# Kernel optimization log

Hardware: AMD Instinct MI355X
Metric: run time of the kernel (lower is better)

## Reference

```python
import jax, jax.numpy as jnp
import numpy as np

N, E = 50000, 800000
F_NODE, F_EDGE, HID, EMB, HEADS = 128, 16, 64, 32, 4
BN_EPS = 1e-5


def _glorot(key, shape):
    fan_in = shape[0] if len(shape) > 1 else shape[-1]
    return jax.random.normal(key, shape, jnp.float32) / np.sqrt(fan_in)


def setup_inputs() -> dict:
    key = jax.random.key(0)
    ks = jax.random.split(key, 32)
    inp = {
        "x": jax.random.normal(ks[0], (N, F_NODE), jnp.float32),
        "edge_attr": jax.random.normal(ks[1], (E, F_EDGE), jnp.float32),
        # GAT layer 0: in=F_NODE, heads=4, C=HID
        "W0": _glorot(ks[2], (F_NODE, HEADS * HID)),
        "We0": _glorot(ks[3], (F_EDGE, HEADS * HID)),
        "as0": _glorot(ks[4], (HEADS, HID)),
        "ad0": _glorot(ks[5], (HEADS, HID)),
        "ae0": _glorot(ks[6], (HEADS, HID)),
        "b0": jnp.zeros((HEADS * HID,), jnp.float32),
        "bn0_g": jnp.ones((HEADS * HID,), jnp.float32),
        "bn0_b": jnp.zeros((HEADS * HID,), jnp.float32),
        # GAT layer 1: in=HEADS*HID, heads=1, C=EMB
        "W1": _glorot(ks[7], (HEADS * HID, EMB)),
        "We1": _glorot(ks[8], (F_EDGE, EMB)),
        "as1": _glorot(ks[9], (1, EMB)),
        "ad1": _glorot(ks[10], (1, EMB)),
        "ae1": _glorot(ks[11], (1, EMB)),
        "b1": jnp.zeros((EMB,), jnp.float32),
        # node decoder: 32 -> 128 -> 64 -> 128
        "ndW1": _glorot(ks[12], (EMB, 2 * HID)),   "ndb1": jnp.zeros((2 * HID,), jnp.float32),
        "nd_g": jnp.ones((2 * HID,), jnp.float32), "nd_b": jnp.zeros((2 * HID,), jnp.float32),
        "ndW2": _glorot(ks[13], (2 * HID, HID)),   "ndb2": jnp.zeros((HID,), jnp.float32),
        "ndW3": _glorot(ks[14], (HID, F_NODE)),    "ndb3": jnp.zeros((F_NODE,), jnp.float32),
        # edge decoder: 2*32+16=80 -> 128 -> 64 -> 1
        "edW1": _glorot(ks[15], (2 * EMB + F_EDGE, 2 * HID)), "edb1": jnp.zeros((2 * HID,), jnp.float32),
        "ed_g": jnp.ones((2 * HID,), jnp.float32), "ed_b": jnp.zeros((2 * HID,), jnp.float32),
        "edW2": _glorot(ks[16], (2 * HID, HID)),   "edb2": jnp.zeros((HID,), jnp.float32),
        "edW3": _glorot(ks[17], (HID, 1)),         "edb3": jnp.zeros((1,), jnp.float32),
        "edge_index": jax.random.randint(ks[18], (2, E), 0, N, jnp.int64),
    }
    return inp


def _bn(x, g, b):
    # eval-mode BatchNorm1d with running mean 0, var 1
    return x / np.sqrt(1.0 + BN_EPS) * g + b


def _gat(x, edge_index, edge_attr, W, b, We, att_s, att_d, att_e, heads, C):
    n = x.shape[0]
    src, dst = edge_index[0], edge_index[1]
    e = edge_attr.shape[0]
    # add self loops; self-loop edge_attr = scatter-mean of incoming edge_attr (PyG fill_value='mean')
    esum = jax.ops.segment_sum(edge_attr, dst, num_segments=n)
    cnt = jax.ops.segment_sum(jnp.ones((e,), edge_attr.dtype), dst, num_segments=n)
    loop_attr = esum / jnp.maximum(cnt, 1.0)[:, None]
    loop = jnp.arange(n, dtype=src.dtype)
    src_f = jnp.concatenate([src, loop])
    dst_f = jnp.concatenate([dst, loop])
    ea = jnp.concatenate([edge_attr, loop_attr], axis=0)
    xw = (x @ W).reshape(n, heads, C)                       # [N,H,C]
    a_s = (xw * att_s).sum(-1)                              # [N,H]
    a_d = (xw * att_d).sum(-1)
    a_e = ((ea @ We).reshape(-1, heads, C) * att_e).sum(-1)  # [E+N,H]
    alpha = jax.nn.leaky_relu(a_s[src_f] + a_d[dst_f] + a_e, 0.2)
    # segment softmax over destination neighborhoods
    m = jax.ops.segment_max(alpha, dst_f, num_segments=n)
    alpha = jnp.exp(alpha - m[dst_f])
    s = jax.ops.segment_sum(alpha, dst_f, num_segments=n)
    alpha = alpha / (s[dst_f] + 1e-16)
    out = jax.ops.segment_sum(alpha[:, :, None] * xw[src_f], dst_f, num_segments=n)
    return out.reshape(n, heads * C) + b


def reference(x, edge_attr, W0, b0, We0, as0, ad0, ae0, bn0_g, bn0_b,
              W1, b1, We1, as1, ad1, ae1,
              ndW1, ndb1, nd_g, nd_b, ndW2, ndb2, ndW3, ndb3,
              edW1, edb1, ed_g, ed_b, edW2, edb2, edW3, edb3,
              edge_index):
    # encoder
    h = _gat(x, edge_index, edge_attr, W0, b0, We0, as0, ad0, ae0, HEADS, HID)
    h = jax.nn.elu(_bn(h, bn0_g, bn0_b))  # residual skipped: 256 != 128; dropout is eval-mode identity
    z = _gat(h, edge_index, edge_attr, W1, b1, We1, as1, ad1, ae1, 1, EMB)
    # node decoder
    n1 = _bn(jax.nn.relu(z @ ndW1 + ndb1), nd_g, nd_b)
    node_recon = jax.nn.relu(n1 @ ndW2 + ndb2) @ ndW3 + ndb3
    # edge decoder
    src, dst = edge_index[0], edge_index[1]
    ef = jnp.concatenate([z[src], z[dst], edge_attr], axis=1)  # [E, 2*EMB+F_EDGE]
    e1 = _bn(jax.nn.relu(ef @ edW1 + edb1), ed_g, ed_b)
    edge_recon = jax.nn.sigmoid((jax.nn.relu(e1 @ edW2 + edb2) @ edW3 + edb3)).squeeze(-1)
    return (z, node_recon, edge_recon)
```

## Files before the change

kernel.cpp:

```cpp
#include <hip/hip_runtime.h>
#include <math.h>

#define BN_K 0.9999950000374997f

static __device__ __forceinline__ float lrelu02(float x) { return x > 0.f ? x : 0.2f * x; }

typedef _Float16 half8 __attribute__((ext_vector_type(8)));
typedef __fp16 fp16x2 __attribute__((ext_vector_type(2)));
typedef float f32x4 __attribute__((ext_vector_type(4)));

static __device__ __forceinline__ unsigned short f2h(float x)
{
    union { _Float16 h; unsigned short u; } q;
    q.h = (_Float16)x;
    return q.u;
}
static __device__ __forceinline__ float h2f(unsigned short u)
{
    union { unsigned short u; _Float16 h; } q;
    q.u = u;
    return (float)q.h;
}
static __device__ __forceinline__ unsigned pkrtz(float a, float b)
{
    union { fp16x2 h; unsigned u; } q;
    q.h = __builtin_amdgcn_cvt_pkrtz(a, b);
    return q.u;
}

__global__ void k_ae_vec(const float* __restrict__ We0, const float* __restrict__ ae0,
                         const float* __restrict__ We1, const float* __restrict__ ae1,
                         const float* __restrict__ edbb, const float* __restrict__ edW2,
                         const float* __restrict__ edb2,
                         float* __restrict__ v0, float* __restrict__ v1,
                         float* __restrict__ b2p)
{
    int t = threadIdx.x;
    if (t < 64) {
        int h = t >> 4, k = t & 15;
        float s = 0.f;
        for (int c = 0; c < 64; ++c) s += We0[k * 256 + h * 64 + c] * ae0[h * 64 + c];
        v0[h * 16 + k] = s;
    } else if (t < 80) {
        int k = t - 64;
        float s = 0.f;
        for (int c = 0; c < 32; ++c) s += We1[k * 32 + c] * ae1[c];
        v1[k] = s;
    } else if (t < 144) {
        int n = t - 80;
        float s = 0.f;
        for (int k = 0; k < 128; ++k) s += edbb[k] * edW2[k * 64 + n];
        b2p[n] = edb2[n] + s;
    }
}

__global__ void k_deg_count(const int* __restrict__ dst, int* __restrict__ deg, int E)
{
    int e = blockIdx.x * blockDim.x + threadIdx.x;
    if (e < E) atomicAdd(&deg[dst[e]], 1);
}

#define SCHUNK 4096
__global__ __launch_bounds__(1024) void k_scan1(const int* __restrict__ deg,
                                                int* __restrict__ rowptr,
                                                int* __restrict__ bsum, int n)
{
    __shared__ int sbuf[1024];
    int b = blockIdx.x, t = threadIdx.x;
    int i0 = b * SCHUNK + t * 4;
    int v[4];
#pragma unroll
    for (int j = 0; j < 4; ++j) v[j] = (i0 + j < n) ? deg[i0 + j] + 1 : 0;
    int s = v[0] + v[1] + v[2] + v[3];
    sbuf[t] = s;
    __syncthreads();
    for (int d = 1; d < 1024; d <<= 1) {
        int tmp = (t >= d) ? sbuf[t - d] : 0;
        __syncthreads();
        sbuf[t] += tmp;
        __syncthreads();
    }
    int run = sbuf[t] - s;
#pragma unroll
    for (int j = 0; j < 4; ++j) {
        run += v[j];
        if (i0 + j < n) rowptr[i0 + j + 1] = run;
    }
    if (t == 1023) bsum[b] = sbuf[1023];
    if (b == 0 && t == 0) rowptr[0] = 0;
}

__global__ void k_scan3(const int* __restrict__ bsum, const int* __restrict__ deg,
                        int* __restrict__ rowptr, int* __restrict__ cur, int n)
{
    int i = blockIdx.x * blockDim.x + threadIdx.x;
    if (i >= n) return;
    int chunk = i / SCHUNK;
    int off = 0;
    for (int b = 0; b < chunk; ++b) off += bsum[b];
    int r = rowptr[i + 1] + off;
    rowptr[i + 1] = r;
    cur[i] = r - (deg[i] + 1);
}

__global__ void k_fill(const int* __restrict__ dst, int* __restrict__ cur,
                       int* __restrict__ col, int E, int N)
{
    int t = blockIdx.x * blockDim.x + threadIdx.x;
    if (t >= E + N) return;
    int d = (t < E) ? dst[t] : (t - E);
    int slot = atomicAdd(&cur[d], 1);
    col[slot] = t;
}

__global__ __launch_bounds__(256) void k_loop_mean(
    const int* __restrict__ rowptr, const int* __restrict__ col,
    const unsigned short* __restrict__ ea16,
    const float* __restrict__ v0, const float* __restrict__ v1,
    float* __restrict__ a_e0, float* __restrict__ a_e1, int N, int E)
{
    int wv = threadIdx.x >> 6, lane = threadIdx.x & 63;
    int i = blockIdx.x * 4 + wv;
    if (i >= N) return;
    int beg = rowptr[i], end = rowptr[i + 1];
    int q = lane >> 4, k = lane & 15;
    float sum = 0.f;
    for (int p = beg + q; p < end; p += 4) {
        int eid = col[p];
        if (eid < E) sum += h2f(ea16[(size_t)eid * 16 + k]);
    }
    sum += __shfl_xor(sum, 16);
    sum += __shfl_xor(sum, 32);
    int cnt = end - beg - 1;
    float mean = sum / (float)max(cnt, 1);
    float p0 = mean * v0[q * 16 + k];
    float p1 = mean * v1[k];
#pragma unroll
    for (int mm = 1; mm < 16; mm <<= 1) { p0 += __shfl_xor(p0, mm); p1 += __shfl_xor(p1, mm); }
    if (k == 0) a_e0[(size_t)(E + i) * 4 + q] = p0;
    if (lane == 0) a_e1[E + i] = p1;
}

__global__ void k_edge_ae(const float* __restrict__ ea,
                          const float* __restrict__ v0, const float* __restrict__ v1,
                          float* __restrict__ a_e0, float* __restrict__ a_e1,
                          unsigned short* __restrict__ ea16, int E)
{
    int idx = blockIdx.x * blockDim.x + threadIdx.x;
    if (idx >= E) return;
    const float* row = ea + (size_t)idx * 16;
    float r[16];
#pragma unroll
    for (int k = 0; k < 16; ++k) r[k] = row[k];
#pragma unroll
    for (int h = 0; h < 4; ++h) {
        float s = 0.f;
#pragma unroll
        for (int k = 0; k < 16; ++k) s = fmaf(r[k], v0[h * 16 + k], s);
        a_e0[(size_t)idx * 4 + h] = s;
    }
    float s1 = 0.f;
#pragma unroll
    for (int k = 0; k < 16; ++k) s1 = fmaf(r[k], v1[k], s1);
    a_e1[idx] = s1;
#pragma unroll
    for (int k = 0; k < 16; k += 4) {
        ushort4 o;
        o.x = f2h(r[k]); o.y = f2h(r[k + 1]); o.z = f2h(r[k + 2]); o.w = f2h(r[k + 3]);
        *(ushort4*)(ea16 + (size_t)idx * 16 + k) = o;
    }
}

__global__ __launch_bounds__(512) void k_pack_all(
    const float* __restrict__ W0, const float* __restrict__ W1,
    const float* __restrict__ nd1, const float* __restrict__ nd2, const float* __restrict__ nd3,
    const float* __restrict__ ed1, const float* __restrict__ ed2,
    const float* __restrict__ edb1, const float* __restrict__ edg,
    unsigned short* __restrict__ pw)
{
    int f = blockIdx.x, t = threadIdx.x;
    int l = t >> 3, i = t & 7, g = l >> 4, m = l & 15;
    float v;
    if (f < 64) {
        int q = f; int k = 32 * (q >> 4) + 8 * g + i, n = 16 * (q & 15) + m;
        v = W0[(size_t)k * 256 + n];
    } else if (f < 80) {
        int q = f - 64; int k = 32 * (q >> 1) + 8 * g + i, n = 16 * (q & 1) + m;
        v = W1[(size_t)k * 32 + n];
    } else if (f < 88) {
        int q = f - 80; int k = 8 * g + i, n = 16 * q + m;
        v = nd1[(size_t)k * 128 + n];
    } else if (f < 104) {
        int q = f - 88; int k = 32 * (q >> 2) + 8 * g + i, n = 16 * (q & 3) + m;
        v = nd2[(size_t)k * 64 + n];
    } else if (f < 120) {
        int q = f - 104; int k = 32 * (q >> 3) + 8 * g + i, n = 16 * (q & 7) + m;
        v = nd3[(size_t)k * 128 + n];
    } else if (f < 144) {
        int q = f - 120; int k = 32 * (q >> 3) + 8 * g + i, n = 16 * (q & 7) + m;
        v = (k < 80) ? ed1[(size_t)k * 128 + n] : (k == 80 ? edb1[n] : 0.f);
    } else {
        int q = f - 144; int k = 32 * (q >> 2) + 8 * g + i, n = 16 * (q & 3) + m;
        v = ed2[(size_t)k * 64 + n] * (edg[k] * BN_K);
    }
    pw[(size_t)f * 512 + t] = f2h(v);
}

template <int KC, int NT, int MODE, int AF32, int NTOT, int DOTS>
__global__ __launch_bounds__(256) void k_gemm16(
    const void* __restrict__ Ain, const unsigned short* __restrict__ pwB,
    void* __restrict__ outp, int M,
    const float* __restrict__ bias, const float* __restrict__ g_,
    const float* __restrict__ bb_,
    const float* __restrict__ attS, const float* __restrict__ attD,
    float* __restrict__ a_sO, float* __restrict__ a_dO)
{
    constexpr int K = KC * 32;
    constexpr int LDA = K + 8;
    __shared__ unsigned short s_pw[KC * NT * 512];
    __shared__ unsigned short s_a[64 * LDA];
    __shared__ float s_c[3 * NT * 16];

    int t = threadIdx.x;
    int ttoff = blockIdx.y * NT;
    for (int idx = t; idx < KC * NT * 64; idx += 256) {
        int f = idx >> 6, e8 = idx & 63;
        int c = f / NT, tt = f - c * NT;
        *(half8*)&s_pw[(size_t)idx * 8] =
            *(const half8*)&pwB[(((size_t)(c * NTOT + ttoff + tt)) * 64 + e8) * 8];
    }
    if (MODE) {
        for (int c = t; c < NT * 16; c += 256) {
            s_c[c] = bias[ttoff * 16 + c];
            if (MODE == 2) {
                s_c[NT * 16 + c] = g_[ttoff * 16 + c] * BN_K;
                s_c[2 * NT * 16 + c] = bb_[ttoff * 16 + c];
            }
        }
    }
    int wv = t >> 6, lane = t & 63, gq = lane >> 4, m = lane & 15;

    float asv[NT], adv[NT];
    if (DOTS) {
#pragma unroll
        for (int tt = 0; tt < NT; ++tt) {
            asv[tt] = attS[ttoff * 16 + 16 * tt + m];
            adv[tt] = attD[ttoff * 16 + 16 * tt + m];
        }
    }

    int nrt = (M + 63) >> 6;
    for (int rt = blockIdx.x; rt < nrt; rt += gridDim.x) {
        int r0 = rt << 6;
        __syncthreads();
        for (int idx = t; idx < 64 * (K / 8); idx += 256) {
            int row = idx / (K / 8), cb = idx % (K / 8);
            half8 v = {};
            if (r0 + row < M) {
                if (AF32) {
                    const float* Af = (const float*)Ain + (size_t)(r0 + row) * K + cb * 8;
                    float4 u0 = *(const float4*)Af;
                    float4 u1 = *(const float4*)(Af + 4);
                    union { half8 h; unsigned u[4]; } q;
                    q.u[0] = pkrtz(u0.x, u0.y); q.u[1] = pkrtz(u0.z, u0.w);
                    q.u[2] = pkrtz(u1.x, u1.y); q.u[3] = pkrtz(u1.z, u1.w);
                    v = q.h;
                } else {
                    v = *(const half8*)&((const unsigned short*)Ain)[(size_t)(r0 + row) * K + cb * 8];
                }
            }
            *(half8*)&s_a[row * LDA + cb * 8] = v;
        }
        __syncthreads();
        f32x4 acc[NT] = {};
#pragma unroll
        for (int c = 0; c < KC; ++c) {
            half8 a = *(half8*)&s_a[(wv * 16 + m) * LDA + 32 * c + 8 * gq];
#pragma unroll
            for (int tt = 0; tt < NT; ++tt) {
                half8 b = *(const half8*)&s_pw[(c * NT + tt) * 512 + lane * 8];
                acc[tt] = __builtin_amdgcn_mfma_f32_16x16x32_f16(a, b, acc[tt], 0, 0, 0);
            }
        }
#pragma unroll
        for (int tt = 0; tt < NT; ++tt) {
            int col = 16 * tt + m;
            int ocol = ttoff * 16 + col;
            float cb = MODE ? s_c[col] : 0.f;
#pragma unroll
            for (int r = 0; r < 4; ++r) {
                int row = r0 + wv * 16 + 4 * gq + r;
                float v = acc[tt][r] + cb;
                if (MODE == 1) v = fmaxf(v, 0.f);
                if (MODE == 2) v = fmaxf(v, 0.f) * s_c[NT * 16 + col] + s_c[2 * NT * 16 + col];
                if (MODE == 3) {
                    if (row < M) ((float*)outp)[(size_t)row * (NTOT * 16) + ocol] = v;
                } else {
                    float o = __shfl_xor(v, 1);
                    if (!(m & 1) && row < M)
                        *(unsigned*)&((unsigned short*)outp)[(size_t)row * (NTOT * 16) + ocol] =
                            pkrtz(v, o);
                }
            }
        }
        if (DOTS == 1) {
#pragma unroll
            for (int r = 0; r < 4; ++r) {
                float psA = 0.f, pdA = 0.f, psB = 0.f, pdB = 0.f;
#pragma unroll
                for (int tt = 0; tt < NT && tt < 4; ++tt) {
                    psA = fmaf(acc[tt][r], asv[tt], psA);
                    pdA = fmaf(acc[tt][r], adv[tt], pdA);
                }
#pragma unroll
                for (int tt = 4; tt < NT; ++tt) {
                    psB = fmaf(acc[tt][r], asv[tt], psB);
                    pdB = fmaf(acc[tt][r], adv[tt], pdB);
                }
#pragma unroll
                for (int mm = 1; mm < 16; mm <<= 1) {
                    psA += __shfl_xor(psA, mm); pdA += __shfl_xor(pdA, mm);
                    psB += __shfl_xor(psB, mm); pdB += __shfl_xor(pdB, mm);
                }
                int row = r0 + wv * 16 + 4 * gq + r;
                if (m == 0 && row < M) {
                    int hA = 2 * blockIdx.y;
                    a_sO[(size_t)row * 4 + hA] = psA; a_sO[(size_t)row * 4 + hA + 1] = psB;
                    a_dO[(size_t)row * 4 + hA] = pdA; a_dO[(size_t)row * 4 + hA + 1] = pdB;
                }
            }
        } else if (DOTS == 2) {
#pragma unroll
            for (int r = 0; r < 4; ++r) {
                float ps = 0.f, pd = 0.f;
#pragma unroll
                for (int tt = 0; tt < NT; ++tt) {
                    ps = fmaf(acc[tt][r], asv[tt], ps);
                    pd = fmaf(acc[tt][r], adv[tt], pd);
                }
#pragma unroll
                for (int mm = 1; mm < 16; mm <<= 1) {
                    ps += __shfl_xor(ps, mm); pd += __shfl_xor(pd, mm);
                }
                int row = r0 + wv * 16 + 4 * gq + r;
                if (m == 0 && row < M) { a_sO[row] = ps; a_dO[row] = pd; }
            }
        }
    }
}

__global__ __launch_bounds__(64) void k_gat0_agg(
    const int* __restrict__ rowptr, const int* __restrict__ col, const int* __restrict__ srcA,
    const float* __restrict__ a_s, const float* __restrict__ a_d, const float* __restrict__ a_e,
    const unsigned short* __restrict__ xw16, const float* __restrict__ b0,
    const float* __restrict__ bng, const float* __restrict__ bnb,
    unsigned short* __restrict__ hout16, int N, int E)
{
    int i = blockIdx.x;
    int lane = threadIdx.x;
    int beg = rowptr[i], end = rowptr[i + 1];
    float ad[4];
#pragma unroll
    for (int h = 0; h < 4; ++h) ad[h] = a_d[(size_t)i * 4 + h];

    float al[4] = {-1e30f, -1e30f, -1e30f, -1e30f};
    int sl0 = i;
    int p0 = beg + lane;
    if (p0 < end) {
        int eid = col[p0];
        sl0 = (eid < E) ? srcA[eid] : i;
        float4 as4 = *(const float4*)(a_s + (size_t)sl0 * 4);
        float4 ae4 = *(const float4*)(a_e + (size_t)eid * 4);
        al[0] = lrelu02(as4.x + ad[0] + ae4.x);
        al[1] = lrelu02(as4.y + ad[1] + ae4.y);
        al[2] = lrelu02(as4.z + ad[2] + ae4.z);
        al[3] = lrelu02(as4.w + ad[3] + ae4.w);
    }
    float mx[4] = {al[0], al[1], al[2], al[3]};
    for (int p = p0 + 64; p < end; p += 64) {
        int eid = col[p];
        int s = (eid < E) ? srcA[eid] : i;
        float4 as4 = *(const float4*)(a_s + (size_t)s * 4);
        float4 ae4 = *(const float4*)(a_e + (size_t)eid * 4);
        mx[0] = fmaxf(mx[0], lrelu02(as4.x + ad[0] + ae4.x));
        mx[1] = fmaxf(mx[1], lrelu02(as4.y + ad[1] + ae4.y));
        mx[2] = fmaxf(mx[2], lrelu02(as4.z + ad[2] + ae4.z));
        mx[3] = fmaxf(mx[3], lrelu02(as4.w + ad[3] + ae4.w));
    }
#pragma unroll
    for (int h = 0; h < 4; ++h)
#pragma unroll
        for (int m = 1; m < 64; m <<= 1) mx[h] = fmaxf(mx[h], __shfl_xor(mx[h], m));

    __shared__ float wls[256];
    __shared__ int s_src[64];
    int hl = lane >> 4;
    float accx = 0.f, accy = 0.f, accz = 0.f, accw = 0.f;
    float s0 = 0.f, s1 = 0.f, s2 = 0.f, s3 = 0.f;
    for (int base = beg; base < end; base += 64) {
        int p = base + lane;
        int cnt = min(64, end - base);
        if (p < end) {
            float aa0, aa1, aa2, aa3;
            int s;
            if (base == beg) {
                s = sl0;
                aa0 = al[0]; aa1 = al[1]; aa2 = al[2]; aa3 = al[3];
            } else {
                int eid = col[p];
                s = (eid < E) ? srcA[eid] : i;
                float4 as4 = *(const float4*)(a_s + (size_t)s * 4);
                float4 ae4 = *(const float4*)(a_e + (size_t)eid * 4);
                aa0 = lrelu02(as4.x + ad[0] + ae4.x);
                aa1 = lrelu02(as4.y + ad[1] + ae4.y);
                aa2 = lrelu02(as4.z + ad[2] + ae4.z);
                aa3 = lrelu02(as4.w + ad[3] + ae4.w);
            }
            float w0 = expf(aa0 - mx[0]);
            float w1 = expf(aa1 - mx[1]);
            float w2 = expf(aa2 - mx[2]);
            float w3 = expf(aa3 - mx[3]);
            s0 += w0; s1 += w1; s2 += w2; s3 += w3;
            wls[lane * 4 + 0] = w0; wls[lane * 4 + 1] = w1;
            wls[lane * 4 + 2] = w2; wls[lane * 4 + 3] = w3;
            s_src[lane] = s;
        }
        __syncthreads();
        int q = 0;
        for (; q + 3 < cnt; q += 4) {
            int ss0 = s_src[q], ss1 = s_src[q + 1], ss2 = s_src[q + 2], ss3 = s_src[q + 3];
            ushort4 x0 = *(const ushort4*)(xw16 + (size_t)ss0 * 256 + lane * 4);
            ushort4 x1 = *(const ushort4*)(xw16 + (size_t)ss1 * 256 + lane * 4);
            ushort4 x2 = *(const ushort4*)(xw16 + (size_t)ss2 * 256 + lane * 4);
            ushort4 x3 = *(const ushort4*)(xw16 + (size_t)ss3 * 256 + lane * 4);
            float w0 = wls[q * 4 + hl], w1 = wls[(q + 1) * 4 + hl];
            float w2 = wls[(q + 2) * 4 + hl], w3 = wls[(q + 3) * 4 + hl];
            accx = fmaf(w0, h2f(x0.x), accx); accy = fmaf(w0, h2f(x0.y), accy);
            accz = fmaf(w0, h2f(x0.z), accz); accw = fmaf(w0, h2f(x0.w), accw);
            accx = fmaf(w1, h2f(x1.x), accx); accy = fmaf(w1, h2f(x1.y), accy);
            accz = fmaf(w1, h2f(x1.z), accz); accw = fmaf(w1, h2f(x1.w), accw);
            accx = fmaf(w2, h2f(x2.x), accx); accy = fmaf(w2, h2f(x2.y), accy);
            accz = fmaf(w2, h2f(x2.z), accz); accw = fmaf(w2, h2f(x2.w), accw);
            accx = fmaf(w3, h2f(x3.x), accx); accy = fmaf(w3, h2f(x3.y), accy);
            accz = fmaf(w3, h2f(x3.z), accz); accw = fmaf(w3, h2f(x3.w), accw);
        }
        for (; q < cnt; ++q) {
            int ss = s_src[q];
            float w = wls[q * 4 + hl];
            ushort4 xv = *(const ushort4*)(xw16 + (size_t)ss * 256 + lane * 4);
            accx = fmaf(w, h2f(xv.x), accx);
            accy = fmaf(w, h2f(xv.y), accy);
            accz = fmaf(w, h2f(xv.z), accz);
            accw = fmaf(w, h2f(xv.w), accw);
        }
        __syncthreads();
    }
#pragma unroll
    for (int m = 1; m < 64; m <<= 1) {
        s0 += __shfl_xor(s0, m); s1 += __shfl_xor(s1, m);
        s2 += __shfl_xor(s2, m); s3 += __shfl_xor(s3, m);
    }
    float sden = ((hl == 0) ? s0 : (hl == 1) ? s1 : (hl == 2) ? s2 : s3) + 1e-16f;

    int ch = lane * 4;
    float out[4] = {accx / sden, accy / sden, accz / sden, accw / sden};
    ushort4 ov;
    unsigned short* po = (unsigned short*)&ov;
#pragma unroll
    for (int j = 0; j < 4; ++j) {
        int c = ch + j;
        float v = out[j] + b0[c];
        v = v * (BN_K * bng[c]) + bnb[c];
        po[j] = f2h((v > 0.f) ? v : expm1f(v));
    }
    *(ushort4*)(hout16 + (size_t)i * 256 + ch) = ov;
}

__global__ __launch_bounds__(64) void k_gat1_agg(
    const int* __restrict__ rowptr, const int* __restrict__ col, const int* __restrict__ srcA,
    const float* __restrict__ a_s, const float* __restrict__ a_d, const float* __restrict__ a_e,
    const unsigned short* __restrict__ xw16, const float* __restrict__ b1,
    float* __restrict__ zout, unsigned short* __restrict__ z16, int N, int E)
{
    int i = blockIdx.x;
    int lane = threadIdx.x;
    int beg = rowptr[i], end = rowptr[i + 1];
    float ad = a_d[i];
    float al = -1e30f;
    int sl0 = i;
    int p0 = beg + lane;
    if (p0 < end) {
        int eid = col[p0];
        sl0 = (eid < E) ? srcA[eid] : i;
        al = lrelu02(a_s[sl0] + ad + a_e[eid]);
    }
    float mx = al;
    for (int p = p0 + 64; p < end; p += 64) {
        int eid = col[p];
        int s = (eid < E) ? srcA[eid] : i;
        mx = fmaxf(mx, lrelu02(a_s[s] + ad + a_e[eid]));
    }
#pragma unroll
    for (int m = 1; m < 64; m <<= 1) mx = fmaxf(mx, __shfl_xor(mx, m));

    __shared__ float wls[64];
    __shared__ int s_src[64];
    float accA = 0.f, accB = 0.f, ssum = 0.f;
    int sub = lane >> 4;
    int ch = (lane & 15) * 2;
    for (int base = beg; base < end; base += 64) {
        int p = base + lane;
        int cnt = min(64, end - base);
        if (p < end) {
            float aa;
            int s;
            if (base == beg) { s = sl0; aa = al; }
            else {
                int eid = col[p];
                s = (eid < E) ? srcA[eid] : i;
                aa = lrelu02(a_s[s] + ad + a_e[eid]);
            }
            float w = expf(aa - mx);
            ssum += w;
            wls[lane] = w;
            s_src[lane] = s;
        }
        __syncthreads();
        int q = sub;
        for (; q + 12 < cnt; q += 16) {
            int ss0 = s_src[q], ss1 = s_src[q + 4], ss2 = s_src[q + 8], ss3 = s_src[q + 12];
            float w0 = wls[q], w1 = wls[q + 4], w2 = wls[q + 8], w3 = wls[q + 12];
            ushort2 x0 = *(const ushort2*)(xw16 + (size_t)ss0 * 32 + ch);
            ushort2 x1 = *(const ushort2*)(xw16 + (size_t)ss1 * 32 + ch);
            ushort2 x2 = *(const ushort2*)(xw16 + (size_t)ss2 * 32 + ch);
            ushort2 x3 = *(const ushort2*)(xw16 + (size_t)ss3 * 32 + ch);
            accA = fmaf(w0, h2f(x0.x), accA); accB = fmaf(w0, h2f(x0.y), accB);
            accA = fmaf(w1, h2f(x1.x), accA); accB = fmaf(w1, h2f(x1.y), accB);
            accA = fmaf(w2, h2f(x2.x), accA); accB = fmaf(w2, h2f(x2.y), accB);
            accA = fmaf(w3, h2f(x3.x), accA); accB = fmaf(w3, h2f(x3.y), accB);
        }
        for (; q < cnt; q += 4) {
            int ss = s_src[q];
            float w = wls[q];
            ushort2 xv = *(const ushort2*)(xw16 + (size_t)ss * 32 + ch);
            accA = fmaf(w, h2f(xv.x), accA);
            accB = fmaf(w, h2f(xv.y), accB);
        }
        __syncthreads();
    }
#pragma unroll
    for (int m = 1; m < 64; m <<= 1) ssum += __shfl_xor(ssum, m);
    accA += __shfl_xor(accA, 16); accB += __shfl_xor(accB, 16);
    accA += __shfl_xor(accA, 32); accB += __shfl_xor(accB, 32);
    if (lane < 16) {
        float inv = 1.f / (ssum + 1e-16f);
        float vA = accA * inv + b1[ch];
        float vB = accB * inv + b1[ch + 1];
        *(float2*)(zout + (size_t)i * 32 + ch) = make_float2(vA, vB);
        *(unsigned*)(z16 + (size_t)i * 32 + ch) = pkrtz(vA, vB);
    }
}

#define H1_STRIDE 136

__global__ __launch_bounds__(256, 3) void k_edge_dec_mfma(
    const unsigned short* __restrict__ z16, const unsigned short* __restrict__ ea16,
    const int* __restrict__ srcA, const int* __restrict__ dstA,
    const unsigned short* __restrict__ pw,
    const float* __restrict__ b2p, const float* __restrict__ w3,
    const float* __restrict__ b3v, float* __restrict__ out, int E)
{
    __shared__ unsigned short s_pw[24 * 512];
    __shared__ unsigned short s_h1[4][16 * H1_STRIDE];

    int t = threadIdx.x;
    for (int idx = t; idx < 1536; idx += 256)
        *(half8*)&s_pw[idx * 8] = *(const half8*)&pw[idx * 8];
    __syncthreads();

    int wv = t >> 6, lane = t & 63;
    int g = lane >> 4, m = lane & 15;
    unsigned short* h1 = s_h1[wv];

    half8 w2r[16];
#pragma unroll
    for (int q = 0; q < 16; ++q)
        w2r[q] = *(const half8*)&pw[(size_t)(24 + q) * 512 + lane * 8];

    float w3t[4], b2t[4];
#pragma unroll
    for (int q = 0; q < 4; ++q) { w3t[q] = w3[16 * q + m]; b2t[q] = b2p[16 * q + m]; }
    float b3 = b3v[0];

    int ntiles = (E + 15) >> 4;
    int gw = blockIdx.x * 4 + wv;
    int nw = gridDim.x * 4;

    half8 a0n = {}, a1n = {}, a2n = {};
    {
        int e = (gw << 4) + m;
        if (gw < ntiles && e < E) {
            int si = srcA[e], di = dstA[e];
            a0n = *(const half8*)&z16[(size_t)si * 32 + 8 * g];
            a1n = *(const half8*)&z16[(size_t)di * 32 + 8 * g];
            if (g < 2) a2n = *(const half8*)&ea16[(size_t)e * 16 + 8 * g];
        }
        if (g == 2) a2n[0] = (_Float16)1.f;
    }

    for (int tile = gw; tile < ntiles; ) {
        half8 a0 = a0n, a1 = a1n, a2 = a2n;
        int e0 = tile << 4;
        int nxt = tile + nw;

        a0n = half8{}; a1n = half8{}; a2n = half8{};
        {
            int e = (nxt << 4) + m;
            if (nxt < ntiles && e < E) {
                int si = srcA[e], di = dstA[e];
                a0n = *(const half8*)&z16[(size_t)si * 32 + 8 * g];
                a1n = *(const half8*)&z16[(size_t)di * 32 + 8 * g];
                if (g < 2) a2n = *(const half8*)&ea16[(size_t)e * 16 + 8 * g];
            }
            if (g == 2) a2n[0] = (_Float16)1.f;
        }

        f32x4 acc1[8] = {};
#pragma unroll
        for (int tt = 0; tt < 8; ++tt)
            acc1[tt] = __builtin_amdgcn_mfma_f32_16x16x32_f16(a0, *(const half8*)&s_pw[(0 * 8 + tt) * 512 + lane * 8], acc1[tt], 0, 0, 0);
#pragma unroll
        for (int tt = 0; tt < 8; ++tt)
            acc1[tt] = __builtin_amdgcn_mfma_f32_16x16x32_f16(a1, *(const half8*)&s_pw[(1 * 8 + tt) * 512 + lane * 8], acc1[tt], 0, 0, 0);
#pragma unroll
        for (int tt = 0; tt < 8; ++tt)
            acc1[tt] = __builtin_amdgcn_mfma_f32_16x16x32_f16(a2, *(const half8*)&s_pw[(2 * 8 + tt) * 512 + lane * 8], acc1[tt], 0, 0, 0);

#pragma unroll
        for (int tt = 0; tt < 8; ++tt) {
#pragma unroll
            for (int r = 0; r < 4; ++r) {
                float v = fmaxf(acc1[tt][r], 0.f);
                float vo = __shfl_xor(v, 1);
                if (!(m & 1))
                    *(unsigned*)&h1[(4 * g + r) * H1_STRIDE + 16 * tt + m] = pkrtz(v, vo);
            }
        }
        asm volatile("s_waitcnt lgkmcnt(0)" ::: "memory");
        __builtin_amdgcn_sched_barrier(0);

        f32x4 acc2[4] = {};
#pragma unroll
        for (int c = 0; c < 4; ++c) {
            half8 a = *(half8*)&h1[m * H1_STRIDE + 32 * c + 8 * g];
#pragma unroll
            for (int tt = 0; tt < 4; ++tt)
                acc2[tt] = __builtin_amdgcn_mfma_f32_16x16x32_f16(a, w2r[c * 4 + tt], acc2[tt], 0, 0, 0);
        }
        float s[4];
#pragma unroll
        for (int r = 0; r < 4; ++r) {
            float acc = 0.f;
#pragma unroll
            for (int tt = 0; tt < 4; ++tt) {
                float v = fmaxf(acc2[tt][r] + b2t[tt], 0.f);
                acc = fmaf(v, w3t[tt], acc);
            }
            acc += __shfl_xor(acc, 1);
            acc += __shfl_xor(acc, 2);
            acc += __shfl_xor(acc, 4);
            acc += __shfl_xor(acc, 8);
            s[r] = acc;
        }
        if (m == 0) {
            int eb = e0 + 4 * g;
            if (eb + 3 < E) {
                float4 o;
                o.x = 1.f / (1.f + expf(-(s[0] + b3)));
                o.y = 1.f / (1.f + expf(-(s[1] + b3)));
                o.z = 1.f / (1.f + expf(-(s[2] + b3)));
                o.w = 1.f / (1.f + expf(-(s[3] + b3)));
                *(float4*)(out + eb) = o;
            } else {
#pragma unroll
                for (int r = 0; r < 4; ++r)
                    if (eb + r < E) out[eb + r] = 1.f / (1.f + expf(-(s[r] + b3)));
            }
        }
        tile = nxt;
    }
}

extern "C" void kernel_launch(void* const* d_in, const int* in_sizes, int n_in,
                              void* d_out, int out_size, void* d_ws, size_t ws_size,
                              hipStream_t stream)
{
    const float* x    = (const float*)d_in[0];
    const float* ea   = (const float*)d_in[1];
    const float* W0   = (const float*)d_in[2];
    const float* We0  = (const float*)d_in[3];
    const float* as0  = (const float*)d_in[4];
    const float* ad0  = (const float*)d_in[5];
    const float* ae0  = (const float*)d_in[6];
    const float* b0   = (const float*)d_in[7];
    const float* bn0g = (const float*)d_in[8];
    const float* bn0b = (const float*)d_in[9];
    const float* W1   = (const float*)d_in[10];
    const float* We1  = (const float*)d_in[11];
    const float* as1  = (const float*)d_in[12];
    const float* ad1  = (const float*)d_in[13];
    const float* ae1  = (const float*)d_in[14];
    const float* b1   = (const float*)d_in[15];
    const float* ndW1 = (const float*)d_in[16];
    const float* ndb1 = (const float*)d_in[17];
    const float* ndg  = (const float*)d_in[18];
    const float* ndbb = (const float*)d_in[19];
    const float* ndW2 = (const float*)d_in[20];
    const float* ndb2 = (const float*)d_in[21];
    const float* ndW3 = (const float*)d_in[22];
    const float* ndb3 = (const float*)d_in[23];
    const float* edW1 = (const float*)d_in[24];
    const float* edb1 = (const float*)d_in[25];
    const float* edg  = (const float*)d_in[26];
    const float* edbb = (const float*)d_in[27];
    const float* edW2 = (const float*)d_in[28];
    const float* edb2 = (const float*)d_in[29];
    const float* edW3 = (const float*)d_in[30];
    const float* edb3 = (const float*)d_in[31];
    const int*   eidx = (const int*)d_in[32];

    const int N = in_sizes[0] / 128;
    const int E = in_sizes[1] / 16;
    const int* srcA = eidx;
    const int* dstA = eidx + E;

    char* ws = (char*)d_ws;
    size_t o = 0;
    auto alloc = [&](size_t bytes) -> void* {
        void* p = ws + o;
        o = (o + bytes + 255) & ~(size_t)255;
        return p;
    };
    typedef unsigned short u16;
    u16*   xw0_16 = (u16*)alloc((size_t)N * 256 * 2);
    u16*   hbuf16 = (u16*)alloc((size_t)N * 256 * 2);
    u16*   xw1_16 = (u16*)alloc((size_t)N * 32 * 2);
    u16*   z16    = (u16*)alloc((size_t)N * 32 * 2);
    u16*   n1_16  = (u16*)alloc((size_t)N * 128 * 2);
    u16*   h2n16  = (u16*)alloc((size_t)N * 64 * 2);
    u16*   ea16   = (u16*)alloc((size_t)E * 16 * 2);
    float* a_s0   = (float*)alloc((size_t)N * 4 * 4);
    float* a_d0   = (float*)alloc((size_t)N * 4 * 4);
    float* a_e0a  = (float*)alloc((size_t)(E + N) * 4 * 4);
    float* a_e1a  = (float*)alloc((size_t)(E + N) * 4);
    float* a_s1   = (float*)alloc((size_t)N * 4);
    float* a_d1   = (float*)alloc((size_t)N * 4);
    int*   deg    = (int*)alloc((size_t)N * 4);
    int*   rowptr = (int*)alloc((size_t)(N + 1) * 4);
    int*   cur    = (int*)alloc((size_t)N * 4);
    int*   col    = (int*)alloc((size_t)(E + N) * 4);
    int*   bsum   = (int*)alloc(64 * 4);
    float* v0     = (float*)alloc(64 * 4);
    float* v1     = (float*)alloc(16 * 4);
    float* b2p    = (float*)alloc(64 * 4);
    u16*   pw     = (u16*)alloc((size_t)160 * 512 * 2);

    float* z_out    = (float*)d_out;
    float* node_out = z_out + (size_t)N * 32;
    float* edge_out = node_out + (size_t)N * 128;

    const int nb = (N + SCHUNK - 1) / SCHUNK;
    const int nrt = (N + 63) / 64;

    hipMemsetAsync(deg, 0, (size_t)N * 4, stream);
    k_pack_all<<<160, 512, 0, stream>>>(W0, W1, ndW1, ndW2, ndW3, edW1, edW2, edb1, edg, pw);
    k_ae_vec<<<1, 192, 0, stream>>>(We0, ae0, We1, ae1, edbb, edW2, edb2, v0, v1, b2p);
    k_deg_count<<<(E + 255) / 256, 256, 0, stream>>>(dstA, deg, E);
    k_scan1<<<nb, 1024, 0, stream>>>(deg, rowptr, bsum, N);
    k_scan3<<<(N + 255) / 256, 256, 0, stream>>>(bsum, deg, rowptr, cur, N);
    k_fill<<<(E + N + 255) / 256, 256, 0, stream>>>(dstA, cur, col, E, N);
    k_edge_ae<<<(E + 255) / 256, 256, 0, stream>>>(ea, v0, v1, a_e0a, a_e1a, ea16, E);
    k_loop_mean<<<(N + 3) / 4, 256, 0, stream>>>(rowptr, col, ea16, v0, v1, a_e0a, a_e1a, N, E);

    k_gemm16<4, 8, 0, 1, 16, 1><<<dim3(nrt, 2), 256, 0, stream>>>(
        x, pw, xw0_16, N, nullptr, nullptr, nullptr, as0, ad0, a_s0, a_d0);
    k_gat0_agg<<<N, 64, 0, stream>>>(rowptr, col, srcA, a_s0, a_d0, a_e0a, xw0_16, b0, bn0g, bn0b,
                                     hbuf16, N, E);

    k_gemm16<8, 2, 0, 0, 2, 2><<<dim3(nrt, 1), 256, 0, stream>>>(
        hbuf16, pw + (size_t)64 * 512, xw1_16, N, nullptr, nullptr, nullptr,
        as1, ad1, a_s1, a_d1);
    k_gat1_agg<<<N, 64, 0, stream>>>(rowptr, col, srcA, a_s1, a_d1, a_e1a, xw1_16, b1,
                                     z_out, z16, N, E);

    k_gemm16<1, 8, 2, 0, 8, 0><<<dim3(nrt, 1), 256, 0, stream>>>(
        z16, pw + (size_t)80 * 512, n1_16, N, ndb1, ndg, ndbb, nullptr, nullptr, nullptr, nullptr);
    k_gemm16<4, 4, 1, 0, 4, 0><<<dim3(nrt, 1), 256, 0, stream>>>(
        n1_16, pw + (size_t)88 * 512, h2n16, N, ndb2, nullptr, nullptr, nullptr, nullptr, nullptr, nullptr);
    k_gemm16<2, 8, 3, 0, 8, 0><<<dim3(nrt, 1), 256, 0, stream>>>(
        h2n16, pw + (size_t)104 * 512, node_out, N, ndb3, nullptr, nullptr, nullptr, nullptr, nullptr, nullptr);

    k_edge_dec_mfma<<<768, 256, 0, stream>>>(z16, ea16, srcA, dstA, pw + (size_t)120 * 512,
                                             b2p, edW3, edb3, edge_out, E);
}
```

Baseline: 424.9 us.

## Fuse node decoder MLP into one MFMA kernel and merge setup kernels

Replaces the three node-decoder GEMM launches with a single persistent kernel that keeps intermediate n1 and h2 activations in shared memory as fp16 and chains three MFMA stages per 64-row tile. Also folds the degree-count atomics into the edge attention-prep kernel and moves the small attention-vector precompute into an extra block of the weight pack kernel. This removes global round-trips for the 128- and 64-wide intermediates and several launches, at the cost of heavier shared memory use (lower occupancy) in the fused kernel.

```diff
diff --git a/kernel.cpp b/kernel.cpp
--- a/kernel.cpp
+++ b/kernel.cpp
@@ -26,38 +26,6 @@
     union { fp16x2 h; unsigned u; } q;
     q.h = __builtin_amdgcn_cvt_pkrtz(a, b);
     return q.u;
-}
-
-__global__ void k_ae_vec(const float* __restrict__ We0, const float* __restrict__ ae0,
-                         const float* __restrict__ We1, const float* __restrict__ ae1,
-                         const float* __restrict__ edbb, const float* __restrict__ edW2,
-                         const float* __restrict__ edb2,
-                         float* __restrict__ v0, float* __restrict__ v1,
-                         float* __restrict__ b2p)
-{
-    int t = threadIdx.x;
-    if (t < 64) {
-        int h = t >> 4, k = t & 15;
-        float s = 0.f;
-        for (int c = 0; c < 64; ++c) s += We0[k * 256 + h * 64 + c] * ae0[h * 64 + c];
-        v0[h * 16 + k] = s;
-    } else if (t < 80) {
-        int k = t - 64;
-        float s = 0.f;
-        for (int c = 0; c < 32; ++c) s += We1[k * 32 + c] * ae1[c];
-        v1[k] = s;
-    } else if (t < 144) {
-        int n = t - 80;
-        float s = 0.f;
-        for (int k = 0; k < 128; ++k) s += edbb[k] * edW2[k * 64 + n];
-        b2p[n] = edb2[n] + s;
-    }
-}
-
-__global__ void k_deg_count(const int* __restrict__ dst, int* __restrict__ deg, int E)
-{
-    int e = blockIdx.x * blockDim.x + threadIdx.x;
-    if (e < E) atomicAdd(&deg[dst[e]], 1);
 }
 
 #define SCHUNK 4096
@@ -143,11 +111,13 @@
 
 __global__ void k_edge_ae(const float* __restrict__ ea,
                           const float* __restrict__ v0, const float* __restrict__ v1,
+                          const int* __restrict__ dstA, int* __restrict__ deg,
                           float* __restrict__ a_e0, float* __restrict__ a_e1,
                           unsigned short* __restrict__ ea16, int E)
 {
     int idx = blockIdx.x * blockDim.x + threadIdx.x;
     if (idx >= E) return;
+    atomicAdd(&deg[dstA[idx]], 1);
     const float* row = ea + (size_t)idx * 16;
     float r[16];
 #pragma unroll
@@ -176,9 +146,32 @@
     const float* __restrict__ nd1, const float* __restrict__ nd2, const float* __restrict__ nd3,
     const float* __restrict__ ed1, const float* __restrict__ ed2,
     const float* __restrict__ edb1, const float* __restrict__ edg,
-    unsigned short* __restrict__ pw)
+    const float* __restrict__ We0, const float* __restrict__ ae0,
+    const float* __restrict__ We1, const float* __restrict__ ae1,
+    const float* __restrict__ edbb, const float* __restrict__ edb2,
+    unsigned short* __restrict__ pw,
+    float* __restrict__ v0, float* __restrict__ v1, float* __restrict__ b2p)
 {
     int f = blockIdx.x, t = threadIdx.x;
+    if (f == 160) {
+        if (t < 64) {
+            int h = t >> 4, k = t & 15;
+            float s = 0.f;
+            for (int c = 0; c < 64; ++c) s += We0[k * 256 + h * 64 + c] * ae0[h * 64 + c];
+            v0[h * 16 + k] = s;
+        } else if (t < 80) {
+            int k = t - 64;
+            float s = 0.f;
+            for (int c = 0; c < 32; ++c) s += We1[k * 32 + c] * ae1[c];
+            v1[k] = s;
+        } else if (t < 144) {
+            int n = t - 80;
+            float s = 0.f;
+            for (int k = 0; k < 128; ++k) s += edbb[k] * ed2[k * 64 + n];
+            b2p[n] = edb2[n] + s;
+        }
+        return;
+    }
     int l = t >> 3, i = t & 7, g = l >> 4, m = l & 15;
     float v;
     if (f < 64) {
@@ -558,6 +551,119 @@
         float vB = accB * inv + b1[ch + 1];
         *(float2*)(zout + (size_t)i * 32 + ch) = make_float2(vA, vB);
         *(unsigned*)(z16 + (size_t)i * 32 + ch) = pkrtz(vA, vB);
+    }
+}
+
+#define N1_STRIDE 136
+#define H2_STRIDE 72
+
+__global__ __launch_bounds__(256, 2) void k_node_dec(
+    const unsigned short* __restrict__ z16, const unsigned short* __restrict__ pw,
+    const float* __restrict__ b1, const float* __restrict__ g1, const float* __restrict__ bb1,
+    const float* __restrict__ b2, const float* __restrict__ b3,
+    float* __restrict__ out, int N)
+{
+    __shared__ unsigned short s_pw[40 * 512];
+    __shared__ unsigned short s_z[64 * 40];
+    __shared__ unsigned short s_n1[4][16 * N1_STRIDE];
+    __shared__ unsigned short s_h2[4][16 * H2_STRIDE];
+    __shared__ float s_c[128 * 3 + 64 + 128];
+
+    int t = threadIdx.x;
+    for (int idx = t; idx < 2560; idx += 256)
+        *(half8*)&s_pw[idx * 8] = *(const half8*)&pw[idx * 8];
+    if (t < 128) {
+        s_c[t] = b1[t];
+        s_c[128 + t] = g1[t] * BN_K;
+        s_c[256 + t] = bb1[t];
+        s_c[448 + t] = b3[t];
+    }
+    if (t < 64) s_c[384 + t] = b2[t];
+    __syncthreads();
+
+    int wv = t >> 6, lane = t & 63;
+    int g = lane >> 4, m = lane & 15;
+    unsigned short* n1 = s_n1[wv];
+    unsigned short* h2 = s_h2[wv];
+
+    int nrt = (N + 63) >> 6;
+    for (int rt = blockIdx.x; rt < nrt; rt += gridDim.x) {
+        int r0 = rt << 6;
+        __syncthreads();
+        {
+            int row = t >> 2, cb = t & 3;
+            half8 v = {};
+            if (r0 + row < N) v = *(const half8*)&z16[(size_t)(r0 + row) * 32 + cb * 8];
+            *(half8*)&s_z[row * 40 + cb * 8] = v;
+        }
+        __syncthreads();
+
+        f32x4 acc1[8] = {};
+        {
+            half8 a = *(half8*)&s_z[(wv * 16 + m) * 40 + 8 * g];
+#pragma unroll
+            for (int tt = 0; tt < 8; ++tt)
+                acc1[tt] = __builtin_amdgcn_mfma_f32_16x16x32_f16(
+                    a, *(const half8*)&s_pw[tt * 512 + lane * 8], acc1[tt], 0, 0, 0);
+        }
+#pragma unroll
+        for (int tt = 0; tt < 8; ++tt) {
+            int col = 16 * tt + m;
+            float cb = s_c[col], cg = s_c[128 + col], cbb = s_c[256 + col];
+#pragma unroll
+            for (int r = 0; r < 4; ++r) {
+                float v = fmaxf(acc1[tt][r] + cb, 0.f) * cg + cbb;
+                float vo = __shfl_xor(v, 1);
+                if (!(m & 1))
+                    *(unsigned*)&n1[(4 * g + r) * N1_STRIDE + 16 * tt + m] = pkrtz(v, vo);
+            }
+        }
+        asm volatile("s_waitcnt lgkmcnt(0)" ::: "memory");
+        __builtin_amdgcn_sched_barrier(0);
+
+        f32x4 acc2[4] = {};
+#pragma unroll
+        for (int c = 0; c < 4; ++c) {
+            half8 a = *(half8*)&n1[m * N1_STRIDE + 32 * c + 8 * g];
+#pragma unroll
+            for (int tt = 0; tt < 4; ++tt)
+                acc2[tt] = __builtin_amdgcn_mfma_f32_16x16x32_f16(
+                    a, *(const half8*)&s_pw[(8 + c * 4 + tt) * 512 + lane * 8], acc2[tt], 0, 0, 0);
+        }
+#pragma unroll
+        for (int tt = 0; tt < 4; ++tt) {
+            int col = 16 * tt + m;
+            float cb = s_c[384 + col];
+#pragma unroll
+            for (int r = 0; r < 4; ++r) {
+                float v = fmaxf(acc2[tt][r] + cb, 0.f);
+                float vo = __shfl_xor(v, 1);
+                if (!(m & 1))
+                    *(unsigned*)&h2[(4 * g + r) * H2_STRIDE + 16 * tt + m] = pkrtz(v, vo);
+            }
+        }
+        asm volatile("s_waitcnt lgkmcnt(0)" ::: "memory");
+        __builtin_amdgcn_sched_barrier(0);
+
+        f32x4 acc3[8] = {};
+#pragma unroll
+        for (int c = 0; c < 2; ++c) {
+            half8 a = *(half8*)&h2[m * H2_STRIDE + 32 * c + 8 * g];
+#pragma unroll
+            for (int tt = 0; tt < 8; ++tt)
+                acc3[tt] = __builtin_amdgcn_mfma_f32_16x16x32_f16(
+                    a, *(const half8*)&s_pw[(24 + c * 8 + tt) * 512 + lane * 8], acc3[tt], 0, 0, 0);
+        }
+#pragma unroll
+        for (int tt = 0; tt < 8; ++tt) {
+            int col = 16 * tt + m;
+            float cb = s_c[448 + col];
+#pragma unroll
+            for (int r = 0; r < 4; ++r) {
+                int row = r0 + wv * 16 + 4 * g + r;
+                if (row < N) out[(size_t)row * 128 + col] = acc3[tt][r] + cb;
+            }
+        }
     }
 }
 
@@ -746,8 +852,6 @@
     u16*   hbuf16 = (u16*)alloc((size_t)N * 256 * 2);
     u16*   xw1_16 = (u16*)alloc((size_t)N * 32 * 2);
     u16*   z16    = (u16*)alloc((size_t)N * 32 * 2);
-    u16*   n1_16  = (u16*)alloc((size_t)N * 128 * 2);
-    u16*   h2n16  = (u16*)alloc((size_t)N * 64 * 2);
     u16*   ea16   = (u16*)alloc((size_t)E * 16 * 2);
     float* a_s0   = (float*)alloc((size_t)N * 4 * 4);
     float* a_d0   = (float*)alloc((size_t)N * 4 * 4);
@@ -773,13 +877,12 @@
     const int nrt = (N + 63) / 64;
 
     hipMemsetAsync(deg, 0, (size_t)N * 4, stream);
-    k_pack_all<<<160, 512, 0, stream>>>(W0, W1, ndW1, ndW2, ndW3, edW1, edW2, edb1, edg, pw);
-    k_ae_vec<<<1, 192, 0, stream>>>(We0, ae0, We1, ae1, edbb, edW2, edb2, v0, v1, b2p);
-    k_deg_count<<<(E + 255) / 256, 256, 0, stream>>>(dstA, deg, E);
+    k_pack_all<<<161, 512, 0, stream>>>(W0, W1, ndW1, ndW2, ndW3, edW1, edW2, edb1, edg,
+                                        We0, ae0, We1, ae1, edbb, edb2, pw, v0, v1, b2p);
+    k_edge_ae<<<(E + 255) / 256, 256, 0, stream>>>(ea, v0, v1, dstA, deg, a_e0a, a_e1a, ea16, E);
     k_scan1<<<nb, 1024, 0, stream>>>(deg, rowptr, bsum, N);
     k_scan3<<<(N + 255) / 256, 256, 0, stream>>>(bsum, deg, rowptr, cur, N);
     k_fill<<<(E + N + 255) / 256, 256, 0, stream>>>(dstA, cur, col, E, N);
-    k_edge_ae<<<(E + 255) / 256, 256, 0, stream>>>(ea, v0, v1, a_e0a, a_e1a, ea16, E);
     k_loop_mean<<<(N + 3) / 4, 256, 0, stream>>>(rowptr, col, ea16, v0, v1, a_e0a, a_e1a, N, E);
 
     k_gemm16<4, 8, 0, 1, 16, 1><<<dim3(nrt, 2), 256, 0, stream>>>(
@@ -793,12 +896,8 @@
     k_gat1_agg<<<N, 64, 0, stream>>>(rowptr, col, srcA, a_s1, a_d1, a_e1a, xw1_16, b1,
                                      z_out, z16, N, E);
 
-    k_gemm16<1, 8, 2, 0, 8, 0><<<dim3(nrt, 1), 256, 0, stream>>>(
-        z16, pw + (size_t)80 * 512, n1_16, N, ndb1, ndg, ndbb, nullptr, nullptr, nullptr, nullptr);
-    k_gemm16<4, 4, 1, 0, 4, 0><<<dim3(nrt, 1), 256, 0, stream>>>(
-        n1_16, pw + (size_t)88 * 512, h2n16, N, ndb2, nullptr, nullptr, nullptr, nullptr, nullptr, nullptr);
-    k_gemm16<2, 8, 3, 0, 8, 0><<<dim3(nrt, 1), 256, 0, stream>>>(
-        h2n16, pw + (size_t)104 * 512, node_out, N, ndb3, nullptr, nullptr, nullptr, nullptr, nullptr, nullptr);
+    k_node_dec<<<512, 256, 0, stream>>>(z16, pw + (size_t)80 * 512,
+                                        ndb1, ndg, ndbb, ndb2, ndb3, node_out, N);
 
     k_edge_dec_mfma<<<768, 256, 0, stream>>>(z16, ea16, srcA, dstA, pw + (size_t)120 * 512,
                                              b2p, edW3, edb3, edge_out, E);
```

Result: faster. 405.4 us (-4.6%).
